# Kernel optimization log

Hardware: AMD Instinct MI355X
Metric: run time of the kernel (lower is better)

## Reference

```python
import jax, jax.numpy as jnp
import numpy as np
import math

N = 50000
E = 800000
HID = 128
HEADS = 8
DK = HID // HEADS
EPS_LN = 1e-5


def setup_inputs() -> dict:
    key = jax.random.key(0)
    ks = jax.random.split(key, 20)
    s = 1.0 / math.sqrt(HID)
    inp = {
        'x': jax.random.normal(ks[0], (N, HID), jnp.float32),
        'Wq': jax.random.normal(ks[1], (HID, HID), jnp.float32) * s,
        'bq': jnp.zeros((HID,), jnp.float32),
        'Wk': jax.random.normal(ks[2], (HID, HID), jnp.float32) * s,
        'bk': jnp.zeros((HID,), jnp.float32),
        'Wv': jax.random.normal(ks[3], (HID, HID), jnp.float32) * s,
        'bv': jnp.zeros((HID,), jnp.float32),
        'Wo': jax.random.normal(ks[4], (HID, HID), jnp.float32) * s,
        'bo': jnp.zeros((HID,), jnp.float32),
        'ln1_g': jnp.ones((HID,), jnp.float32),
        'ln1_b': jnp.zeros((HID,), jnp.float32),
        'W1': jax.random.normal(ks[5], (HID, 4 * HID), jnp.float32) * s,
        'b1': jnp.zeros((4 * HID,), jnp.float32),
        'W2': jax.random.normal(ks[6], (4 * HID, HID), jnp.float32) * (0.5 * s),
        'b2': jnp.zeros((HID,), jnp.float32),
        'ln2_g': jnp.ones((HID,), jnp.float32),
        'ln2_b': jnp.zeros((HID,), jnp.float32),
        'edge_index': jax.random.randint(ks[7], (2, E), 0, N, jnp.int64 if jax.config.jax_enable_x64 else jnp.int32),
    }
    return inp


def _layer_norm(x, g, b):
    mu = jnp.mean(x, axis=-1, keepdims=True)
    var = jnp.mean(jnp.square(x - mu), axis=-1, keepdims=True)
    return (x - mu) * jax.lax.rsqrt(var + EPS_LN) * g + b


def reference(x, Wq, bq, Wk, bk, Wv, bv, Wo, bo, ln1_g, ln1_b, W1, b1, W2, b2, ln2_g, ln2_b, edge_index):
    n = x.shape[0]
    src, tgt = edge_index[0], edge_index[1]
    Q = (x @ Wq + bq).reshape(n, HEADS, DK)
    K = (x @ Wk + bk).reshape(n, HEADS, DK)
    V = (x @ Wv + bv).reshape(n, HEADS, DK)
    # per-edge scores: (E, H)
    scores = jnp.sum(Q[tgt] * K[src], axis=-1) / math.sqrt(DK)
    # segment softmax over incoming edges of each target node
    smax = jax.ops.segment_max(scores, tgt, num_segments=n)  # (N, H), -inf for empty
    sexp = jnp.exp(scores - smax[tgt])
    ssum = jax.ops.segment_sum(sexp, tgt, num_segments=n)
    alpha = sexp / (ssum[tgt] + 1e-16)  # (E, H)
    # weighted V aggregation
    messages = alpha[:, :, None] * V[src]  # (E, H, DK)
    agg = jax.ops.segment_sum(messages, tgt, num_segments=n).reshape(n, HID)
    out = agg @ Wo + bo
    h = _layer_norm(x + out, ln1_g, ln1_b)
    ff = jax.nn.relu(h @ W1 + b1) @ W2 + b2
    return _layer_norm(h + ff, ln2_g, ln2_b)
```

## Files before the change

kernel.cpp:

```cpp
#include <hip/hip_runtime.h>
#include <math.h>

typedef __attribute__((ext_vector_type(8))) short bf16x8;
typedef __attribute__((ext_vector_type(4))) float f32x4;

__device__ __forceinline__ unsigned short f2b(float f) {
    unsigned int u = __float_as_uint(f);
    unsigned int r = (u + 0x7fffu + ((u >> 16) & 1u)) >> 16;
    return (unsigned short)r;
}
__device__ __forceinline__ float blo(unsigned int w) { return __uint_as_float(w << 16); }
__device__ __forceinline__ float bhi(unsigned int w) { return __uint_as_float(w & 0xffff0000u); }
__device__ __forceinline__ float b2f(unsigned short u) { return __uint_as_float((unsigned int)u << 16); }

__device__ __forceinline__ void gload_lds16(const void* g, void* lds) {
    __builtin_amdgcn_global_load_lds(
        (const __attribute__((address_space(1))) unsigned int*)g,
        (__attribute__((address_space(3))) unsigned int*)lds, 16, 0, 0);
}

template<int K, int EPI>
__global__ __launch_bounds__(256)
void mfma_gemm(const unsigned short* __restrict__ A,
               const unsigned short* __restrict__ BT,
               const float* __restrict__ bias,
               const void* __restrict__ res,
               const float* __restrict__ lng,
               const float* __restrict__ lnb,
               void* __restrict__ outv, int M, int NC)
{
    __shared__ unsigned short As[128 * 64];
    __shared__ unsigned short Bs[128 * 64];
    const int tid  = threadIdx.x;
    const int lane = tid & 63;
    const int wid  = tid >> 6;
    const int wr = wid >> 1, wc = wid & 1;
    const int rowBase = blockIdx.x * 128;
    const int colBase = blockIdx.y * 128;

    f32x4 acc[4][4];
#pragma unroll
    for (int i = 0; i < 4; ++i)
#pragma unroll
        for (int j = 0; j < 4; ++j) acc[i][j] = (f32x4)0.f;

    int srow[4], skoff[4];
#pragma unroll
    for (int t = 0; t < 4; ++t) {
        int c = tid + t * 256;
        int r = c >> 3, cc = c & 7;
        srow[t]  = r;
        skoff[t] = ((cc ^ (r & 7)) << 3);
    }

    const int rl = lane & 15;
    const int kh = lane >> 4;

    for (int k0 = 0; k0 < K; k0 += 64) {
#pragma unroll
        for (int t = 0; t < 4; ++t) {
            int c = tid + t * 256;
            gload_lds16(A + (size_t)(rowBase + srow[t]) * K + k0 + skoff[t], &As[c * 8]);
            gload_lds16(BT + (size_t)(colBase + srow[t]) * K + k0 + skoff[t], &Bs[c * 8]);
        }
        __syncthreads();

        bf16x8 a[4][2], b[4][2];
#pragma unroll
        for (int mi = 0; mi < 4; ++mi)
#pragma unroll
            for (int kt = 0; kt < 2; ++kt) {
                a[mi][kt] = *(const bf16x8*)&As[(((wr * 64 + mi * 16 + rl) * 64) + kt * 32 + kh * 8) ^ ((rl & 7) << 3)];
                b[mi][kt] = *(const bf16x8*)&Bs[(((wc * 64 + mi * 16 + rl) * 64) + kt * 32 + kh * 8) ^ ((rl & 7) << 3)];
            }
#pragma unroll
        for (int kt = 0; kt < 2; ++kt)
#pragma unroll
            for (int mi = 0; mi < 4; ++mi)
#pragma unroll
                for (int ni = 0; ni < 4; ++ni)
                    acc[mi][ni] = __builtin_amdgcn_mfma_f32_16x16x32_bf16(a[mi][kt], b[ni][kt], acc[mi][ni], 0, 0, 0);
        __syncthreads();
    }

    if (EPI == 3 || EPI == 4) {
        float* ls = (float*)As;
        float bb[4], gg[4], be[4];
#pragma unroll
        for (int ni = 0; ni < 4; ++ni) {
            int col = wc * 64 + ni * 16 + rl;
            bb[ni] = bias[col];
            gg[ni] = lng[col];
            be[ni] = lnb[col];
        }
#pragma unroll
        for (int mi = 0; mi < 4; ++mi) {
#pragma unroll
            for (int r = 0; r < 4; ++r) {
                int lrow = wr * 64 + mi * 16 + kh * 4 + r;
                int row  = rowBase + lrow;
                float s = 0.f, ss = 0.f;
#pragma unroll
                for (int ni = 0; ni < 4; ++ni) {
                    int col = wc * 64 + ni * 16 + rl;
                    float rr = 0.f;
                    if (row < M) {
                        if (EPI == 3) rr = ((const float*)res)[(size_t)row * 128 + col];
                        else          rr = b2f(((const unsigned short*)res)[(size_t)row * 128 + col]);
                    }
                    float v = acc[mi][ni][r] + bb[ni] + rr;
                    acc[mi][ni][r] = v;
                    s += v; ss += v * v;
                }
#pragma unroll
                for (int off = 1; off < 16; off <<= 1) {
                    s  += __shfl_xor(s,  off, 64);
                    ss += __shfl_xor(ss, off, 64);
                }
                if (rl == 0) {
                    ls[lrow * 2 + wc]       = s;
                    ls[256 + lrow * 2 + wc] = ss;
                }
            }
        }
        __syncthreads();
#pragma unroll
        for (int mi = 0; mi < 4; ++mi) {
#pragma unroll
            for (int r = 0; r < 4; ++r) {
                int lrow = wr * 64 + mi * 16 + kh * 4 + r;
                int row  = rowBase + lrow;
                float s  = ls[lrow * 2] + ls[lrow * 2 + 1];
                float ss = ls[256 + lrow * 2] + ls[256 + lrow * 2 + 1];
                float mean = s * (1.f / 128.f);
                float var  = ss * (1.f / 128.f) - mean * mean;
                float rstd = rsqrtf(var + 1e-5f);
#pragma unroll
                for (int ni = 0; ni < 4; ++ni) {
                    int col = wc * 64 + ni * 16 + rl;
                    float o = (acc[mi][ni][r] - mean) * rstd * gg[ni] + be[ni];
                    if (EPI == 3) {
                        ((unsigned short*)outv)[(size_t)row * 128 + col] = (row < M) ? f2b(o) : (unsigned short)0;
                    } else {
                        if (row < M) ((float*)outv)[(size_t)row * 128 + col] = o;
                    }
                }
            }
        }
    } else {
#pragma unroll
        for (int ni = 0; ni < 4; ++ni) {
            const int col = colBase + wc * 64 + ni * 16 + rl;
            const float bv = bias[col];
#pragma unroll
            for (int mi = 0; mi < 4; ++mi) {
                const int rowb = rowBase + wr * 64 + mi * 16 + kh * 4;
#pragma unroll
                for (int r = 0; r < 4; ++r) {
                    float v = acc[mi][ni][r] + bv;
                    if (EPI == 1) v = fmaxf(v, 0.f);
                    ((unsigned short*)outv)[(size_t)(rowb + r) * NC + col] = f2b(v);
                }
            }
        }
    }
}

__global__ void cast_all(const float* __restrict__ x, unsigned short* __restrict__ xb,
                         int n, int npad, int xblocks,
                         const float* __restrict__ Wq, const float* __restrict__ Wk,
                         const float* __restrict__ Wv, const float* __restrict__ Wo,
                         const float* __restrict__ W1, const float* __restrict__ W2,
                         const float* __restrict__ bq, const float* __restrict__ bk,
                         const float* __restrict__ bv,
                         unsigned short* __restrict__ WcatT, unsigned short* __restrict__ WoT,
                         unsigned short* __restrict__ W1T, unsigned short* __restrict__ W2T,
                         float* __restrict__ bqkv, int* __restrict__ bcnt)
{
    if (blockIdx.x < (unsigned)xblocks) {
        size_t i = ((size_t)blockIdx.x * 256 + threadIdx.x) * 4;
        if (i >= (size_t)npad * 128) return;
        float4 v = make_float4(0.f, 0.f, 0.f, 0.f);
        if (i < (size_t)n * 128) v = *(const float4*)(x + i);
        ushort4 o;
        o.x = f2b(v.x); o.y = f2b(v.y); o.z = f2b(v.z); o.w = f2b(v.w);
        *(ushort4*)(xb + i) = o;
        return;
    }
    int i = (blockIdx.x - xblocks) * 256 + threadIdx.x;
    if (i < 49152) {
        int j = i >> 7, k = i & 127;
        const float* W = (j < 128) ? Wq : ((j < 256) ? Wk : Wv);
        WcatT[i] = f2b(W[k * 128 + (j & 127)]);
    } else if (i < 65536) {
        int t = i - 49152; int j = t >> 7, k = t & 127;
        WoT[t] = f2b(Wo[k * 128 + j]);
    } else if (i < 131072) {
        int t = i - 65536; int j = t >> 7, k = t & 127;
        W1T[t] = f2b(W1[k * 512 + j]);
    } else if (i < 196608) {
        int t = i - 131072; int j = t >> 9, k = t & 511;
        W2T[t] = f2b(W2[k * 128 + j]);
    }
    if (i < 384) bqkv[i] = (i < 128) ? bq[i] : ((i < 256) ? bk[i - 128] : bv[i - 256]);
    if (i < 1024) bcnt[i] = 0;
}

#define EPB 8192

__global__ __launch_bounds__(512)
void bucket_count(const int* __restrict__ tgt, int* __restrict__ bcnt, int E, int nb)
{
    __shared__ int hist[1024];
    int base = blockIdx.x * EPB;
    for (int i = threadIdx.x; i < nb; i += 512) hist[i] = 0;
    __syncthreads();
    int end = min(base + EPB, E);
    for (int e = base + threadIdx.x; e < end; e += 512)
        atomicAdd(&hist[tgt[e] >> 6], 1);
    __syncthreads();
    for (int i = threadIdx.x; i < nb; i += 512)
        if (hist[i] > 0) atomicAdd(&bcnt[i], hist[i]);
}

__global__ __launch_bounds__(64)
void bucket_scan(const int* __restrict__ bcnt, int* __restrict__ bstart,
                 int* __restrict__ bcur, int nb, int E)
{
    int lane = threadIdx.x;
    int carry = 0;
    for (int c = 0; c < nb; c += 64) {
        int idx = c + lane;
        int v = (idx < nb) ? bcnt[idx] : 0;
        int orig = v;
#pragma unroll
        for (int off = 1; off < 64; off <<= 1) {
            int y = __shfl_up(v, off, 64);
            if (lane >= off) v += y;
        }
        if (idx < nb) { int ex = carry + v - orig; bstart[idx] = ex; bcur[idx] = ex; }
        carry += __shfl(v, 63, 64);
    }
    if (lane == 0) bstart[nb] = E;
}

__global__ __launch_bounds__(512)
void bucket_group(const int* __restrict__ src, const int* __restrict__ tgt,
                  int* __restrict__ bcur, int2* __restrict__ stage, int E, int nb)
{
    __shared__ int2 eb[EPB];
    __shared__ int hist[1024], lofs[1024], lcur[1024], gbase[1024];
    int base = blockIdx.x * EPB;
    int tid = threadIdx.x;
    for (int i = tid; i < nb; i += 512) { hist[i] = 0; lcur[i] = 0; }
    __syncthreads();
    int end = min(base + EPB, E);
    for (int e = base + tid; e < end; e += 512)
        atomicAdd(&hist[tgt[e] >> 6], 1);
    __syncthreads();
    if (tid < 64) {
        int carry = 0;
        for (int c = 0; c < nb; c += 64) {
            int idx = c + tid;
            int v = (idx < nb) ? hist[idx] : 0;
            int orig = v;
#pragma unroll
            for (int off = 1; off < 64; off <<= 1) {
                int y = __shfl_up(v, off, 64);
                if (tid >= off) v += y;
            }
            if (idx < nb) lofs[idx] = carry + v - orig;
            carry += __shfl(v, 63, 64);
        }
    }
    __syncthreads();
    for (int e = base + tid; e < end; e += 512) {
        int t = tgt[e], b = t >> 6;
        int r = atomicAdd(&lcur[b], 1);
        eb[lofs[b] + r] = make_int2(src[e], t);
    }
    __syncthreads();
    for (int i = tid; i < nb; i += 512)
        if (hist[i] > 0) gbase[i] = atomicAdd(&bcur[i], hist[i]);
    __syncthreads();
    int cnt = end - base;
    for (int i = tid; i < cnt; i += 512) {
        int2 v = eb[i];
        int b = v.y >> 6;
        stage[gbase[b] + (i - lofs[b])] = v;
    }
}

__global__ __launch_bounds__(256)
void bucket_sort(const int2* __restrict__ stage, const int* __restrict__ bstart,
                 int* __restrict__ rowp, int2* __restrict__ epos, int n, int nb)
{
    __shared__ int2 eb[3072], eb2[3072];
    __shared__ int tcnt[64], tofs[64], tcur[64];
    int b = blockIdx.x;
    int t0 = b << 6;
    if (t0 >= n) return;
    int t1 = min(t0 + 64, n);
    int s0 = bstart[b], s1 = bstart[b + 1];
    int cnt = s1 - s0;
    int tid = threadIdx.x;
    if (tid < 64) { tcnt[tid] = 0; tcur[tid] = 0; }
    __syncthreads();
    bool fits = (cnt <= 3072);
    if (fits) {
        for (int i = tid; i < cnt; i += 256) {
            int2 v = stage[s0 + i];
            eb[i] = v;
            atomicAdd(&tcnt[v.y - t0], 1);
        }
    } else {
        for (int i = tid; i < cnt; i += 256)
            atomicAdd(&tcnt[stage[s0 + i].y - t0], 1);
    }
    __syncthreads();
    if (tid < 64) {
        int v = tcnt[tid], orig = v;
#pragma unroll
        for (int off = 1; off < 64; off <<= 1) {
            int y = __shfl_up(v, off, 64);
            if (tid >= off) v += y;
        }
        tofs[tid] = v - orig;
        int t = t0 + tid;
        if (t < t1) rowp[t] = s0 + v - orig;
        if (t == n - 1) rowp[n] = s1;
    }
    __syncthreads();
    if (fits) {
        for (int i = tid; i < cnt; i += 256) {
            int2 v = eb[i];
            int lt = v.y - t0;
            int r = atomicAdd(&tcur[lt], 1);
            eb2[tofs[lt] + r] = v;
        }
        __syncthreads();
        for (int i = tid; i < cnt; i += 256) epos[s0 + i] = eb2[i];
    } else {
        for (int i = tid; i < cnt; i += 256) {
            int2 v = stage[s0 + i];
            int lt = v.y - t0;
            int r = atomicAdd(&tcur[lt], 1);
            epos[s0 + tofs[lt] + r] = v;
        }
    }
}

#define SCORE_SCALE 0.360673760222241f

__global__ __launch_bounds__(256)
void score_kernel(const unsigned short* __restrict__ qkv, const int2* __restrict__ epos,
                  unsigned short* __restrict__ wexp, int E)
{
    int gw = (blockIdx.x * 256 + threadIdx.x) >> 4;
    int el = threadIdx.x & 15;
    if (gw >= E) return;
    int2 st = epos[gw];
    uint4 qv = *(const uint4*)(qkv + (size_t)st.y * 384 + el * 8);
    uint4 kv = *(const uint4*)(qkv + (size_t)st.x * 384 + 128 + el * 8);
    float d;
    d  = blo(qv.x) * blo(kv.x) + bhi(qv.x) * bhi(kv.x);
    d += blo(qv.y) * blo(kv.y) + bhi(qv.y) * bhi(kv.y);
    d += blo(qv.z) * blo(kv.z) + bhi(qv.z) * bhi(kv.z);
    d += blo(qv.w) * blo(kv.w) + bhi(qv.w) * bhi(kv.w);
    d += __shfl_xor(d, 1, 64);
    if ((el & 1) == 0)
        wexp[(size_t)gw * 8 + (el >> 1)] = f2b(exp2f(d * SCORE_SCALE));
}

__global__ __launch_bounds__(256)
void attn_agg(const unsigned short* __restrict__ qkv, const int* __restrict__ rowp,
              const int2* __restrict__ epos, const unsigned short* __restrict__ wexp,
              unsigned short* __restrict__ agg, int n, int npad)
{
    int wid  = (blockIdx.x * blockDim.x + threadIdx.x) >> 6;
    int lane = threadIdx.x & 63;
    if (wid >= npad) return;
    if (wid >= n) { *(unsigned int*)(agg + (size_t)wid * 128 + lane * 2) = 0u; return; }

    const int head = lane >> 3;
    int e = rowp[wid];
    const int e1 = rowp[wid + 1];

    float s = 0.f, a0 = 0.f, a1 = 0.f;

    for (; e + 8 <= e1; e += 8) {
        int sx[8];
        float w[8];
        unsigned int v[8];
#pragma unroll
        for (int u = 0; u < 8; ++u) sx[u] = epos[e + u].x;
#pragma unroll
        for (int u = 0; u < 8; ++u) w[u] = b2f(wexp[(size_t)(e + u) * 8 + head]);
#pragma unroll
        for (int u = 0; u < 8; ++u)
            v[u] = *(const unsigned int*)(qkv + (size_t)sx[u] * 384 + 256 + lane * 2);
#pragma unroll
        for (int u = 0; u < 8; ++u) {
            s  += w[u];
            a0 += w[u] * blo(v[u]);
            a1 += w[u] * bhi(v[u]);
        }
    }
    for (; e + 4 <= e1; e += 4) {
        int s0 = epos[e].x, s1 = epos[e + 1].x, s2 = epos[e + 2].x, s3 = epos[e + 3].x;
        float w0 = b2f(wexp[(size_t)e * 8 + head]);
        float w1 = b2f(wexp[(size_t)(e + 1) * 8 + head]);
        float w2 = b2f(wexp[(size_t)(e + 2) * 8 + head]);
        float w3 = b2f(wexp[(size_t)(e + 3) * 8 + head]);
        unsigned int v0 = *(const unsigned int*)(qkv + (size_t)s0 * 384 + 256 + lane * 2);
        unsigned int v1 = *(const unsigned int*)(qkv + (size_t)s1 * 384 + 256 + lane * 2);
        unsigned int v2 = *(const unsigned int*)(qkv + (size_t)s2 * 384 + 256 + lane * 2);
        unsigned int v3 = *(const unsigned int*)(qkv + (size_t)s3 * 384 + 256 + lane * 2);
        s  += (w0 + w1) + (w2 + w3);
        a0 += (w0 * blo(v0) + w1 * blo(v1)) + (w2 * blo(v2) + w3 * blo(v3));
        a1 += (w0 * bhi(v0) + w1 * bhi(v1)) + (w2 * bhi(v2) + w3 * bhi(v3));
    }
    for (; e < e1; ++e) {
        int sx = epos[e].x;
        float w = b2f(wexp[(size_t)e * 8 + head]);
        unsigned int vw = *(const unsigned int*)(qkv + (size_t)sx * 384 + 256 + lane * 2);
        s  += w;
        a0 += w * blo(vw);
        a1 += w * bhi(vw);
    }
    float inv = 1.f / (s + 1e-16f);
    unsigned int o = (unsigned int)f2b(a0 * inv) | ((unsigned int)f2b(a1 * inv) << 16);
    *(unsigned int*)(agg + (size_t)wid * 128 + lane * 2) = o;
}

extern "C" void kernel_launch(void* const* d_in, const int* in_sizes, int n_in,
                              void* d_out, int out_size, void* d_ws, size_t ws_size,
                              hipStream_t stream)
{
    const float* x    = (const float*)d_in[0];
    const float* Wq   = (const float*)d_in[1];
    const float* bq   = (const float*)d_in[2];
    const float* Wk   = (const float*)d_in[3];
    const float* bk   = (const float*)d_in[4];
    const float* Wv   = (const float*)d_in[5];
    const float* bv   = (const float*)d_in[6];
    const float* Wo   = (const float*)d_in[7];
    const float* bo   = (const float*)d_in[8];
    const float* ln1g = (const float*)d_in[9];
    const float* ln1b = (const float*)d_in[10];
    const float* W1   = (const float*)d_in[11];
    const float* b1   = (const float*)d_in[12];
    const float* W2   = (const float*)d_in[13];
    const float* b2   = (const float*)d_in[14];
    const float* ln2g = (const float*)d_in[15];
    const float* ln2b = (const float*)d_in[16];
    const int*   eidx = (const int*)d_in[17];

    const int N_ = in_sizes[0] / 128;
    const int E_ = in_sizes[17] / 2;
    const int Mpad = ((N_ + 127) / 128) * 128;
    const int nb = (N_ + 63) >> 6;
    const int* srcE = eidx;
    const int* tgtE = eidx + E_;
    float* out = (float*)d_out;

    unsigned short* xb   = (unsigned short*)d_ws;
    unsigned short* qkvb = xb + (size_t)Mpad * 128;
    unsigned short* tb   = xb;
    unsigned short* aggb = qkvb + (size_t)Mpad * 384;
    unsigned short* hb   = aggb + (size_t)Mpad * 128;
    unsigned short* wexp = hb + (size_t)Mpad * 128;
    unsigned short* WcatT = wexp + (size_t)E_ * 8;
    unsigned short* WoT  = WcatT + 384 * 128;
    unsigned short* W1T  = WoT + 128 * 128;
    unsigned short* W2T  = W1T + 512 * 128;
    float* bqkv          = (float*)(W2T + 128 * 512);
    int2* stage          = (int2*)(bqkv + 384);
    int2* epos           = stage + E_;
    int* bcnt   = (int*)(epos + E_);
    int* bstart = bcnt + 1024;
    int* bcur   = bstart + 1025;
    int* rowp   = bcur + 1024;

    const int xblocks = (int)(((size_t)Mpad * 128 / 4 + 255) / 256);
    const int gblocks = (E_ + EPB - 1) / EPB;

    cast_all<<<xblocks + 768, 256, 0, stream>>>(x, xb, N_, Mpad, xblocks,
                                                Wq, Wk, Wv, Wo, W1, W2, bq, bk, bv,
                                                WcatT, WoT, W1T, W2T, bqkv, bcnt);

    mfma_gemm<128, 2><<<dim3(Mpad / 128, 3), 256, 0, stream>>>(
        xb, WcatT, bqkv, nullptr, nullptr, nullptr, qkvb, N_, 384);

    bucket_count<<<gblocks, 512, 0, stream>>>(tgtE, bcnt, E_, nb);
    bucket_scan<<<1, 64, 0, stream>>>(bcnt, bstart, bcur, nb, E_);
    bucket_group<<<gblocks, 512, 0, stream>>>(srcE, tgtE, bcur, stage, E_, nb);
    bucket_sort<<<nb, 256, 0, stream>>>(stage, bstart, rowp, epos, N_, nb);

    score_kernel<<<((size_t)E_ * 16 + 255) / 256, 256, 0, stream>>>(qkvb, epos, wexp, E_);
    attn_agg<<<(Mpad + 3) / 4, 256, 0, stream>>>(qkvb, rowp, epos, wexp, aggb, N_, Mpad);

    mfma_gemm<128, 3><<<dim3(Mpad / 128, 1), 256, 0, stream>>>(
        aggb, WoT, bo, x, ln1g, ln1b, hb, N_, 128);

    mfma_gemm<128, 1><<<dim3(Mpad / 128, 4), 256, 0, stream>>>(
        hb, W1T, b1, nullptr, nullptr, nullptr, tb, N_, 512);

    mfma_gemm<512, 4><<<dim3(Mpad / 128, 1), 256, 0, stream>>>(
        tb, W2T, b2, hb, ln2g, ln2b, out, N_, 128);
}
```

Before: 208.0 us.

## Pack edge src/tgt into 32-bit words and fold bucket scan into consumers

Edge records are packed as 16-bit source and target indices in one 32-bit word, which halves the staging and sorted-edge traffic. The separate single-block scan kernel is removed, and each group and sort block redoes the prefix scan of bucket counts locally. The attention aggregation unroll grows from 8 to 16, and the first layer-norm residual now reads bf16 x instead of fp32. The packing assumes node ids fit in 16 bits, but N=50000 fits. The bf16 residual costs some precision, and every block now does a redundant 1024-entry scan.

Result: slower. 214.0 us (+2.9%).

```diff
diff --git a/kernel.cpp b/kernel.cpp
--- a/kernel.cpp
+++ b/kernel.cpp
@@ -24,7 +24,7 @@
 void mfma_gemm(const unsigned short* __restrict__ A,
                const unsigned short* __restrict__ BT,
                const float* __restrict__ bias,
-               const void* __restrict__ res,
+               const unsigned short* __restrict__ res,
                const float* __restrict__ lng,
                const float* __restrict__ lnb,
                void* __restrict__ outv, int M, int NC)
@@ -104,10 +104,7 @@
                 for (int ni = 0; ni < 4; ++ni) {
                     int col = wc * 64 + ni * 16 + rl;
                     float rr = 0.f;
-                    if (row < M) {
-                        if (EPI == 3) rr = ((const float*)res)[(size_t)row * 128 + col];
-                        else          rr = b2f(((const unsigned short*)res)[(size_t)row * 128 + col]);
-                    }
+                    if (row < M) rr = b2f(res[(size_t)row * 128 + col]);
                     float v = acc[mi][ni][r] + bb[ni] + rr;
                     acc[mi][ni][r] = v;
                     s += v; ss += v * v;
@@ -203,7 +200,7 @@
         W2T[t] = f2b(W2[k * 128 + j]);
     }
     if (i < 384) bqkv[i] = (i < 128) ? bq[i] : ((i < 256) ? bk[i - 128] : bv[i - 256]);
-    if (i < 1024) bcnt[i] = 0;
+    if (i < 2048) bcnt[i] = 0;
 }
 
 #define EPB 8192
@@ -223,99 +220,88 @@
         if (hist[i] > 0) atomicAdd(&bcnt[i], hist[i]);
 }
 
-__global__ __launch_bounds__(64)
-void bucket_scan(const int* __restrict__ bcnt, int* __restrict__ bstart,
-                 int* __restrict__ bcur, int nb, int E)
-{
-    int lane = threadIdx.x;
-    int carry = 0;
-    for (int c = 0; c < nb; c += 64) {
-        int idx = c + lane;
-        int v = (idx < nb) ? bcnt[idx] : 0;
-        int orig = v;
-#pragma unroll
-        for (int off = 1; off < 64; off <<= 1) {
-            int y = __shfl_up(v, off, 64);
-            if (lane >= off) v += y;
-        }
-        if (idx < nb) { int ex = carry + v - orig; bstart[idx] = ex; bcur[idx] = ex; }
-        carry += __shfl(v, 63, 64);
-    }
-    if (lane == 0) bstart[nb] = E;
-}
-
-__global__ __launch_bounds__(512)
-void bucket_group(const int* __restrict__ src, const int* __restrict__ tgt,
-                  int* __restrict__ bcur, int2* __restrict__ stage, int E, int nb)
-{
-    __shared__ int2 eb[EPB];
-    __shared__ int hist[1024], lofs[1024], lcur[1024], gbase[1024];
-    int base = blockIdx.x * EPB;
-    int tid = threadIdx.x;
-    for (int i = tid; i < nb; i += 512) { hist[i] = 0; lcur[i] = 0; }
-    __syncthreads();
-    int end = min(base + EPB, E);
-    for (int e = base + tid; e < end; e += 512)
-        atomicAdd(&hist[tgt[e] >> 6], 1);
-    __syncthreads();
+__device__ __forceinline__ void scan1024(const int* __restrict__ src, int* dst,
+                                         int nb, int tid)
+{
     if (tid < 64) {
         int carry = 0;
         for (int c = 0; c < nb; c += 64) {
             int idx = c + tid;
-            int v = (idx < nb) ? hist[idx] : 0;
+            int v = (idx < nb) ? src[idx] : 0;
             int orig = v;
 #pragma unroll
             for (int off = 1; off < 64; off <<= 1) {
                 int y = __shfl_up(v, off, 64);
                 if (tid >= off) v += y;
             }
-            if (idx < nb) lofs[idx] = carry + v - orig;
+            if (idx < nb) dst[idx] = carry + v - orig;
             carry += __shfl(v, 63, 64);
         }
     }
+}
+
+__global__ __launch_bounds__(512)
+void bucket_group(const int* __restrict__ src, const int* __restrict__ tgt,
+                  const int* __restrict__ bcnt, int* __restrict__ bcur,
+                  unsigned int* __restrict__ stage, int E, int nb)
+{
+    __shared__ unsigned int eb[EPB];
+    __shared__ int hist[1024], lofs[1024], lcur[1024], gbase[1024], bst[1024];
+    int base = blockIdx.x * EPB;
+    int tid = threadIdx.x;
+    for (int i = tid; i < nb; i += 512) { hist[i] = 0; lcur[i] = 0; }
+    __syncthreads();
+    int end = min(base + EPB, E);
+    for (int e = base + tid; e < end; e += 512)
+        atomicAdd(&hist[tgt[e] >> 6], 1);
+    __syncthreads();
+    scan1024(hist, lofs, nb, tid);
+    scan1024(bcnt, bst, nb, tid);
     __syncthreads();
     for (int e = base + tid; e < end; e += 512) {
         int t = tgt[e], b = t >> 6;
         int r = atomicAdd(&lcur[b], 1);
-        eb[lofs[b] + r] = make_int2(src[e], t);
+        eb[lofs[b] + r] = ((unsigned int)src[e] << 16) | (unsigned int)t;
     }
     __syncthreads();
     for (int i = tid; i < nb; i += 512)
-        if (hist[i] > 0) gbase[i] = atomicAdd(&bcur[i], hist[i]);
+        if (hist[i] > 0) gbase[i] = bst[i] + atomicAdd(&bcur[i], hist[i]);
     __syncthreads();
     int cnt = end - base;
     for (int i = tid; i < cnt; i += 512) {
-        int2 v = eb[i];
-        int b = v.y >> 6;
+        unsigned int v = eb[i];
+        int b = (v & 0xFFFFu) >> 6;
         stage[gbase[b] + (i - lofs[b])] = v;
     }
 }
 
 __global__ __launch_bounds__(256)
-void bucket_sort(const int2* __restrict__ stage, const int* __restrict__ bstart,
-                 int* __restrict__ rowp, int2* __restrict__ epos, int n, int nb)
-{
-    __shared__ int2 eb[3072], eb2[3072];
+void bucket_sort(const unsigned int* __restrict__ stage, const int* __restrict__ bcnt,
+                 int* __restrict__ rowp, unsigned int* __restrict__ spk, int n, int nb)
+{
+    __shared__ unsigned int eb[3072], eb2[3072];
+    __shared__ int bst[1024];
     __shared__ int tcnt[64], tofs[64], tcur[64];
     int b = blockIdx.x;
     int t0 = b << 6;
     if (t0 >= n) return;
     int t1 = min(t0 + 64, n);
-    int s0 = bstart[b], s1 = bstart[b + 1];
+    int tid = threadIdx.x;
+    scan1024(bcnt, bst, nb, tid);
+    if (tid < 64) { tcnt[tid] = 0; tcur[tid] = 0; }
+    __syncthreads();
+    int s0 = bst[b], s1 = s0 + bcnt[b];
     int cnt = s1 - s0;
-    int tid = threadIdx.x;
-    if (tid < 64) { tcnt[tid] = 0; tcur[tid] = 0; }
-    __syncthreads();
     bool fits = (cnt <= 3072);
     if (fits) {
         for (int i = tid; i < cnt; i += 256) {
-            int2 v = stage[s0 + i];
+            unsigned int v = stage[s0 + i];
             eb[i] = v;
-            atomicAdd(&tcnt[v.y - t0], 1);
+            atomicAdd(&tcnt[(v & 0xFFFFu) - t0], 1);
         }
     } else {
         for (int i = tid; i < cnt; i += 256)
-            atomicAdd(&tcnt[stage[s0 + i].y - t0], 1);
+            atomicAdd(&tcnt[(stage[s0 + i] & 0xFFFFu) - t0], 1);
     }
     __syncthreads();
     if (tid < 64) {
@@ -333,19 +319,19 @@
     __syncthreads();
     if (fits) {
         for (int i = tid; i < cnt; i += 256) {
-            int2 v = eb[i];
-            int lt = v.y - t0;
+            unsigned int v = eb[i];
+            int lt = (v & 0xFFFFu) - t0;
             int r = atomicAdd(&tcur[lt], 1);
             eb2[tofs[lt] + r] = v;
         }
         __syncthreads();
-        for (int i = tid; i < cnt; i += 256) epos[s0 + i] = eb2[i];
+        for (int i = tid; i < cnt; i += 256) spk[s0 + i] = eb2[i];
     } else {
         for (int i = tid; i < cnt; i += 256) {
-            int2 v = stage[s0 + i];
-            int lt = v.y - t0;
+            unsigned int v = stage[s0 + i];
+            int lt = (v & 0xFFFFu) - t0;
             int r = atomicAdd(&tcur[lt], 1);
-            epos[s0 + tofs[lt] + r] = v;
+            spk[s0 + tofs[lt] + r] = v;
         }
     }
 }
@@ -353,15 +339,16 @@
 #define SCORE_SCALE 0.360673760222241f
 
 __global__ __launch_bounds__(256)
-void score_kernel(const unsigned short* __restrict__ qkv, const int2* __restrict__ epos,
+void score_kernel(const unsigned short* __restrict__ qkv, const unsigned int* __restrict__ spk,
                   unsigned short* __restrict__ wexp, int E)
 {
     int gw = (blockIdx.x * 256 + threadIdx.x) >> 4;
     int el = threadIdx.x & 15;
     if (gw >= E) return;
-    int2 st = epos[gw];
-    uint4 qv = *(const uint4*)(qkv + (size_t)st.y * 384 + el * 8);
-    uint4 kv = *(const uint4*)(qkv + (size_t)st.x * 384 + 128 + el * 8);
+    unsigned int st = spk[gw];
+    int srcn = st >> 16, tgtn = st & 0xFFFFu;
+    uint4 qv = *(const uint4*)(qkv + (size_t)tgtn * 384 + el * 8);
+    uint4 kv = *(const uint4*)(qkv + (size_t)srcn * 384 + 128 + el * 8);
     float d;
     d  = blo(qv.x) * blo(kv.x) + bhi(qv.x) * bhi(kv.x);
     d += blo(qv.y) * blo(kv.y) + bhi(qv.y) * bhi(kv.y);
@@ -374,7 +361,7 @@
 
 __global__ __launch_bounds__(256)
 void attn_agg(const unsigned short* __restrict__ qkv, const int* __restrict__ rowp,
-              const int2* __restrict__ epos, const unsigned short* __restrict__ wexp,
+              const unsigned int* __restrict__ spk, const unsigned short* __restrict__ wexp,
               unsigned short* __restrict__ agg, int n, int npad)
 {
     int wid  = (blockIdx.x * blockDim.x + threadIdx.x) >> 6;
@@ -388,26 +375,26 @@
 
     float s = 0.f, a0 = 0.f, a1 = 0.f;
 
-    for (; e + 8 <= e1; e += 8) {
-        int sx[8];
-        float w[8];
-        unsigned int v[8];
-#pragma unroll
-        for (int u = 0; u < 8; ++u) sx[u] = epos[e + u].x;
-#pragma unroll
-        for (int u = 0; u < 8; ++u) w[u] = b2f(wexp[(size_t)(e + u) * 8 + head]);
-#pragma unroll
-        for (int u = 0; u < 8; ++u)
+    for (; e + 16 <= e1; e += 16) {
+        int sx[16];
+        float w[16];
+        unsigned int v[16];
+#pragma unroll
+        for (int u = 0; u < 16; ++u) sx[u] = spk[e + u] >> 16;
+#pragma unroll
+        for (int u = 0; u < 16; ++u) w[u] = b2f(wexp[(size_t)(e + u) * 8 + head]);
+#pragma unroll
+        for (int u = 0; u < 16; ++u)
             v[u] = *(const unsigned int*)(qkv + (size_t)sx[u] * 384 + 256 + lane * 2);
 #pragma unroll
-        for (int u = 0; u < 8; ++u) {
+        for (int u = 0; u < 16; ++u) {
             s  += w[u];
             a0 += w[u] * blo(v[u]);
             a1 += w[u] * bhi(v[u]);
         }
     }
     for (; e + 4 <= e1; e += 4) {
-        int s0 = epos[e].x, s1 = epos[e + 1].x, s2 = epos[e + 2].x, s3 = epos[e + 3].x;
+        int s0 = spk[e] >> 16, s1 = spk[e + 1] >> 16, s2 = spk[e + 2] >> 16, s3 = spk[e + 3] >> 16;
         float w0 = b2f(wexp[(size_t)e * 8 + head]);
         float w1 = b2f(wexp[(size_t)(e + 1) * 8 + head]);
         float w2 = b2f(wexp[(size_t)(e + 2) * 8 + head]);
@@ -421,7 +408,7 @@
         a1 += (w0 * bhi(v0) + w1 * bhi(v1)) + (w2 * bhi(v2) + w3 * bhi(v3));
     }
     for (; e < e1; ++e) {
-        int sx = epos[e].x;
+        int sx = spk[e] >> 16;
         float w = b2f(wexp[(size_t)e * 8 + head]);
         unsigned int vw = *(const unsigned int*)(qkv + (size_t)sx * 384 + 256 + lane * 2);
         s  += w;
@@ -475,11 +462,10 @@
     unsigned short* W1T  = WoT + 128 * 128;
     unsigned short* W2T  = W1T + 512 * 128;
     float* bqkv          = (float*)(W2T + 128 * 512);
-    int2* stage          = (int2*)(bqkv + 384);
-    int2* epos           = stage + E_;
-    int* bcnt   = (int*)(epos + E_);
-    int* bstart = bcnt + 1024;
-    int* bcur   = bstart + 1025;
+    unsigned int* stage  = (unsigned int*)(bqkv + 384);
+    unsigned int* spk    = stage + E_;
+    int* bcnt   = (int*)(spk + E_);
+    int* bcur   = bcnt + 1024;
     int* rowp   = bcur + 1024;
 
     const int xblocks = (int)(((size_t)Mpad * 128 / 4 + 255) / 256);
@@ -493,15 +479,14 @@
         xb, WcatT, bqkv, nullptr, nullptr, nullptr, qkvb, N_, 384);
 
     bucket_count<<<gblocks, 512, 0, stream>>>(tgtE, bcnt, E_, nb);
-    bucket_scan<<<1, 64, 0, stream>>>(bcnt, bstart, bcur, nb, E_);
-    bucket_group<<<gblocks, 512, 0, stream>>>(srcE, tgtE, bcur, stage, E_, nb);
-    bucket_sort<<<nb, 256, 0, stream>>>(stage, bstart, rowp, epos, N_, nb);
-
-    score_kernel<<<((size_t)E_ * 16 + 255) / 256, 256, 0, stream>>>(qkvb, epos, wexp, E_);
-    attn_agg<<<(Mpad + 3) / 4, 256, 0, stream>>>(qkvb, rowp, epos, wexp, aggb, N_, Mpad);
+    bucket_group<<<gblocks, 512, 0, stream>>>(srcE, tgtE, bcnt, bcur, stage, E_, nb);
+    bucket_sort<<<nb, 256, 0, stream>>>(stage, bcnt, rowp, spk, N_, nb);
+
+    score_kernel<<<((size_t)E_ * 16 + 255) / 256, 256, 0, stream>>>(qkvb, spk, wexp, E_);
+    attn_agg<<<(Mpad + 3) / 4, 256, 0, stream>>>(qkvb, rowp, spk, wexp, aggb, N_, Mpad);
 
     mfma_gemm<128, 3><<<dim3(Mpad / 128, 1), 256, 0, stream>>>(
-        aggb, WoT, bo, x, ln1g, ln1b, hb, N_, 128);
+        aggb, WoT, bo, xb, ln1g, ln1b, hb, N_, 128);
 
     mfma_gemm<128, 1><<<dim3(Mpad / 128, 4), 256, 0, stream>>>(
         hb, W1T, b1, nullptr, nullptr, nullptr, tb, N_, 512);
```
